# Performance work log

Hardware: AMD Instinct MI355X
Metric: run time of the kernel (lower is better)

## Reference

```python
import jax, jax.numpy as jnp
import numpy as np

N_NODES = 100000
IN_DIM = 128
HIDDEN = 256
N_CLASSES = 16
N_EDGES = 1600000
N_GRAPHS = 64


def setup_inputs() -> dict:
    key = jax.random.key(0)
    ks = jax.random.split(key, 12)
    x = jax.random.normal(ks[0], (N_NODES, IN_DIM), dtype=jnp.float32)
    edge_index = jax.random.randint(ks[1], (2, N_EDGES), 0, N_NODES, dtype=jnp.int64)
    batch = jnp.sort(jax.random.randint(ks[2], (N_NODES,), 0, N_GRAPHS, dtype=jnp.int64))
    s = 0.05
    # SAGEConv layer 1: lin_l (on aggregated neighbors, with bias), lin_r (on root, no bias)
    W1l = jax.random.normal(ks[3], (IN_DIM, HIDDEN), dtype=jnp.float32) * s
    b1 = jnp.zeros((HIDDEN,), dtype=jnp.float32)
    W1r = jax.random.normal(ks[4], (IN_DIM, HIDDEN), dtype=jnp.float32) * s
    # SAGEConv layer 2
    W2l = jax.random.normal(ks[5], (HIDDEN, HIDDEN), dtype=jnp.float32) * s
    b2 = jnp.zeros((HIDDEN,), dtype=jnp.float32)
    W2r = jax.random.normal(ks[6], (HIDDEN, HIDDEN), dtype=jnp.float32) * s
    # final classifier
    fcW = jax.random.normal(ks[7], (HIDDEN, N_CLASSES), dtype=jnp.float32) * s
    fcb = jnp.zeros((N_CLASSES,), dtype=jnp.float32)
    return {"x": x, "edge_index": edge_index, "batch": batch,
            "W1l": W1l, "b1": b1, "W1r": W1r,
            "W2l": W2l, "b2": b2, "W2r": W2r,
            "fcW": fcW, "fcb": fcb}


def _sage_conv(x, src, dst, Wl, bl, Wr, n_nodes):
    # mean aggregation of neighbor features onto destination nodes
    agg = jax.ops.segment_sum(x[src], dst, num_segments=n_nodes)      # [N, d]
    deg = jax.ops.segment_sum(jnp.ones(src.shape, x.dtype), dst, num_segments=n_nodes)
    mean = agg / jnp.maximum(deg, 1.0)[:, None]
    # out = lin_l(mean_neighbors) + lin_r(x_root)  (PyG SAGEConv, mean aggr)
    return mean @ Wl + bl + x @ Wr


def reference(x, edge_index, batch, W1l, b1, W1r, W2l, b2, W2r, fcW, fcb):
    src, dst = edge_index[0], edge_index[1]
    h = jax.nn.relu(_sage_conv(x, src, dst, W1l, b1, W1r, N_NODES))
    # dropout is identity in inference mode
    h = jax.nn.relu(_sage_conv(h, src, dst, W2l, b2, W2r, N_NODES))
    # global mean pool over graphs in the batch
    g_sum = jax.ops.segment_sum(h, batch, num_segments=N_GRAPHS)      # [G, d]
    g_cnt = jax.ops.segment_sum(jnp.ones(batch.shape, h.dtype), batch, num_segments=N_GRAPHS)
    g = g_sum / jnp.maximum(g_cnt, 1.0)[:, None]
    return g @ fcW + fcb                                              # [G, num_classes]
```

## Files before the change

kernel.cpp:

```cpp
#include <hip/hip_runtime.h>

#define INDIM 128
#define HID 256
#define NCLS 16
#define NGRAPH 64
#define CHUNK 8192

typedef __bf16 bf16_t;
typedef bf16_t bf16x8 __attribute__((ext_vector_type(8)));
typedef float f32x4 __attribute__((ext_vector_type(4)));

__device__ __forceinline__ float bfu_lo(unsigned v) {
    union { unsigned i; float f; } u; u.i = v << 16; return u.f;
}
__device__ __forceinline__ float bfu_hi(unsigned v) {
    union { unsigned i; float f; } u; u.i = v & 0xffff0000u; return u.f;
}
__device__ __forceinline__ unsigned short f2bf(float f) {
    union { float f; unsigned i; } u; u.f = f;
    unsigned b = u.i;
    return (unsigned short)((b + 0x7fffu + ((b >> 16) & 1u)) >> 16);
}

typedef __attribute__((address_space(1))) const unsigned gu32_t;
typedef __attribute__((address_space(3))) unsigned lu32_t;
__device__ __forceinline__ void gl_lds16(const void* g, void* l) {
    __builtin_amdgcn_global_load_lds((gu32_t*)g, (lu32_t*)l, 16, 0, 0);
}

__global__ void hist_kernel(const int* __restrict__ dst, int* __restrict__ deg, int E) {
    int e = blockIdx.x * blockDim.x + threadIdx.x;
    if (e < E) atomicAdd(&deg[dst[e]], 1);
}

__global__ void scan1_kernel(const int* __restrict__ deg, int* __restrict__ bsum, int n) {
    __shared__ int s[256];
    int t = threadIdx.x;
    int i = blockIdx.x * 256 + t;
    s[t] = (i < n) ? deg[i] : 0;
    __syncthreads();
    for (int off = 128; off > 0; off >>= 1) {
        if (t < off) s[t] += s[t + off];
        __syncthreads();
    }
    if (t == 0) bsum[blockIdx.x] = s[0];
}

__global__ void scan2_kernel(int* bsum, int nb) {
    __shared__ int s[1024];
    int t = threadIdx.x;
    int v = (t < nb) ? bsum[t] : 0;
    s[t] = v;
    __syncthreads();
    for (int off = 1; off < 1024; off <<= 1) {
        int u = (t >= off) ? s[t - off] : 0;
        __syncthreads();
        s[t] += u;
        __syncthreads();
    }
    if (t < nb) bsum[t] = s[t] - v;
}

__global__ void scan3_kernel(const int* __restrict__ deg, const int* __restrict__ bsum,
                             int* __restrict__ offs, int n) {
    __shared__ int s[256];
    int t = threadIdx.x;
    int i = blockIdx.x * 256 + t;
    int v = (i < n) ? deg[i] : 0;
    s[t] = v;
    __syncthreads();
    for (int off = 1; off < 256; off <<= 1) {
        int u = (t >= off) ? s[t - off] : 0;
        __syncthreads();
        s[t] += u;
        __syncthreads();
    }
    if (i < n) offs[i] = s[t] - v + bsum[blockIdx.x];
}

__global__ void initcur_kernel(const int* __restrict__ offs, int* __restrict__ gcur, int nbuck) {
    int t = blockIdx.x * blockDim.x + threadIdx.x;
    if (t < nbuck) gcur[t] = offs[t << 8];
}

__global__ __launch_bounds__(256) void binA_kernel(const int* __restrict__ src,
                                                   const int* __restrict__ dst,
                                                   int* __restrict__ gcur,
                                                   unsigned* __restrict__ tmp,
                                                   int E, int nbuck) {
    __shared__ int hist[512];
    __shared__ int base[512];
    int t = threadIdx.x;
    int e0 = blockIdx.x * CHUNK;
    int e1 = min(e0 + CHUNK, E);
    for (int i = t; i < nbuck; i += 256) hist[i] = 0;
    __syncthreads();
    for (int e = e0 + t; e < e1; e += 256) atomicAdd(&hist[dst[e] >> 8], 1);
    __syncthreads();
    for (int i = t; i < nbuck; i += 256) {
        int c = hist[i];
        base[i] = (c > 0) ? atomicAdd(&gcur[i], c) : 0;
    }
    __syncthreads();
    for (int e = e0 + t; e < e1; e += 256) {
        int d = dst[e];
        int p = atomicAdd(&base[d >> 8], 1);
        tmp[p] = ((unsigned)(d & 255) << 17) | (unsigned)src[e];
    }
}

__global__ __launch_bounds__(256) void binB_kernel(const unsigned* __restrict__ tmp,
                                                   const int* __restrict__ offs,
                                                   int* __restrict__ srclist, int E, int n) {
    __shared__ int cur[256];
    int b = blockIdx.x;
    int node0 = b << 8;
    int nnodes = min(256, n - node0);
    int t = threadIdx.x;
    if (t < nnodes) cur[t] = offs[node0 + t];
    __syncthreads();
    int ebeg = offs[node0];
    int eend = (node0 + 256 < n) ? offs[node0 + 256] : E;
    for (int e = ebeg + t; e < eend; e += 256) {
        unsigned v = tmp[e];
        int p = atomicAdd(&cur[v >> 17], 1);
        srclist[p] = (int)(v & 0x1FFFFu);
    }
}

__global__ void cast_x_kernel(const float* __restrict__ x, unsigned short* __restrict__ xb,
                              int total4) {
    int idx = blockIdx.x * blockDim.x + threadIdx.x;
    if (idx >= total4) return;
    int i4 = idx * 4;
    float4 v = *(const float4*)(x + i4);
    *(ushort4*)(xb + i4) = make_ushort4(f2bf(v.x), f2bf(v.y), f2bf(v.z), f2bf(v.w));
}

__global__ void wcast1_kernel(const float* __restrict__ Wl, const float* __restrict__ Wr,
                              unsigned short* __restrict__ Bt) {
    int idx = blockIdx.x * blockDim.x + threadIdx.x;
    int n = idx >> 8, k = idx & 255;
    float v = (k < 128) ? Wl[(size_t)k * 256 + n] : Wr[(size_t)(k - 128) * 256 + n];
    Bt[(size_t)n * 256 + k] = f2bf(v);
}

__global__ void wcast2_kernel(const float* __restrict__ Wl, const float* __restrict__ Wr,
                              unsigned short* __restrict__ Bt) {
    int idx = blockIdx.x * blockDim.x + threadIdx.x;
    int n = idx >> 9, k = idx & 511;
    float v = (k < 256) ? Wl[(size_t)k * 256 + n] : Wr[(size_t)(k - 256) * 256 + n];
    Bt[(size_t)n * 512 + k] = f2bf(v);
}

__global__ void agg1_kernel(const unsigned short* __restrict__ xb, const int* __restrict__ srclist,
                            const int* __restrict__ offs, const int* __restrict__ deg,
                            unsigned short* __restrict__ mean, int n) {
    int gid = blockIdx.x * blockDim.x + threadIdx.x;
    int node = gid >> 6, lane = gid & 63;
    if (node >= n) return;
    int st = offs[node], d = deg[node], end = st + d;
    float a0 = 0.f, a1 = 0.f, b0 = 0.f, b1 = 0.f;
    float c0 = 0.f, c1 = 0.f, d0 = 0.f, d1 = 0.f;
    int e = st;
    for (; e + 3 < end; e += 4) {
        int s0 = srclist[e], s1 = srclist[e + 1], s2 = srclist[e + 2], s3 = srclist[e + 3];
        unsigned v0 = *(const unsigned*)(xb + (size_t)s0 * 128 + lane * 2);
        unsigned v1 = *(const unsigned*)(xb + (size_t)s1 * 128 + lane * 2);
        unsigned v2 = *(const unsigned*)(xb + (size_t)s2 * 128 + lane * 2);
        unsigned v3 = *(const unsigned*)(xb + (size_t)s3 * 128 + lane * 2);
        a0 += bfu_lo(v0); a1 += bfu_hi(v0);
        b0 += bfu_lo(v1); b1 += bfu_hi(v1);
        c0 += bfu_lo(v2); c1 += bfu_hi(v2);
        d0 += bfu_lo(v3); d1 += bfu_hi(v3);
    }
    for (; e < end; ++e) {
        unsigned v0 = *(const unsigned*)(xb + (size_t)srclist[e] * 128 + lane * 2);
        a0 += bfu_lo(v0); a1 += bfu_hi(v0);
    }
    float inv = 1.f / fmaxf((float)d, 1.f);
    ushort2 o = make_ushort2(f2bf(((a0 + b0) + (c0 + d0)) * inv),
                             f2bf(((a1 + b1) + (c1 + d1)) * inv));
    *(ushort2*)(mean + (size_t)node * 128 + lane * 2) = o;
}

__global__ void agg2_kernel(const unsigned short* __restrict__ h1, const int* __restrict__ srclist,
                            const int* __restrict__ offs, const int* __restrict__ deg,
                            unsigned short* __restrict__ mean, int n) {
    int gid = blockIdx.x * blockDim.x + threadIdx.x;
    int node = gid >> 6, lane = gid & 63;
    if (node >= n) return;
    int st = offs[node], d = deg[node], end = st + d;
    float a0 = 0, a1 = 0, a2 = 0, a3 = 0, b0 = 0, b1 = 0, b2 = 0, b3 = 0;
    float c0 = 0, c1 = 0, c2 = 0, c3 = 0, e0 = 0, e1 = 0, e2 = 0, e3 = 0;
    int e = st;
    for (; e + 3 < end; e += 4) {
        int s0 = srclist[e], s1 = srclist[e + 1], s2 = srclist[e + 2], s3 = srclist[e + 3];
        uint2 v0 = *(const uint2*)(h1 + (size_t)s0 * 256 + lane * 4);
        uint2 v1 = *(const uint2*)(h1 + (size_t)s1 * 256 + lane * 4);
        uint2 v2 = *(const uint2*)(h1 + (size_t)s2 * 256 + lane * 4);
        uint2 v3 = *(const uint2*)(h1 + (size_t)s3 * 256 + lane * 4);
        a0 += bfu_lo(v0.x); a1 += bfu_hi(v0.x); a2 += bfu_lo(v0.y); a3 += bfu_hi(v0.y);
        b0 += bfu_lo(v1.x); b1 += bfu_hi(v1.x); b2 += bfu_lo(v1.y); b3 += bfu_hi(v1.y);
        c0 += bfu_lo(v2.x); c1 += bfu_hi(v2.x); c2 += bfu_lo(v2.y); c3 += bfu_hi(v2.y);
        e0 += bfu_lo(v3.x); e1 += bfu_hi(v3.x); e2 += bfu_lo(v3.y); e3 += bfu_hi(v3.y);
    }
    for (; e < end; ++e) {
        uint2 v0 = *(const uint2*)(h1 + (size_t)srclist[e] * 256 + lane * 4);
        a0 += bfu_lo(v0.x); a1 += bfu_hi(v0.x); a2 += bfu_lo(v0.y); a3 += bfu_hi(v0.y);
    }
    float inv = 1.f / fmaxf((float)d, 1.f);
    ushort4 o = make_ushort4(f2bf(((a0 + b0) + (c0 + e0)) * inv),
                             f2bf(((a1 + b1) + (c1 + e1)) * inv),
                             f2bf(((a2 + b2) + (c2 + e2)) * inv),
                             f2bf(((a3 + b3) + (c3 + e3)) * inv));
    *(ushort4*)(mean + (size_t)node * 256 + lane * 4) = o;
}

template <int KH>
__global__ __launch_bounds__(256) void gemm_kernel(
        const bf16_t* __restrict__ A1, const bf16_t* __restrict__ A2,
        const bf16_t* __restrict__ Bt, const float* __restrict__ bias,
        unsigned short* __restrict__ H, int M) {
    constexpr int KT = 2 * KH;
    constexpr int NC = KT / 64;
    constexpr int CPH = KH / 64;
    __shared__ unsigned short As[64 * 64];
    int t = threadIdx.x, wave = t >> 6, lane = t & 63;
    int quad = lane >> 4, l16 = lane & 15;
    int row0 = blockIdx.x * 64, n0 = wave * 64;

    f32x4 acc[4][4];
#pragma unroll
    for (int i = 0; i < 4; ++i)
#pragma unroll
        for (int j = 0; j < 4; ++j) acc[i][j] = (f32x4)(0.f);

    int rA = wave * 8 + (lane >> 3);
    int kb = lane & 7;
    int kswA = (kb ^ (rA & 7)) << 3;
    unsigned short* ldsA = &As[(size_t)(wave * 8) * 64];
    unsigned short* ldsB = &As[(size_t)(32 + wave * 8) * 64];

    const bf16_t* Bp = Bt + (size_t)(n0 + l16) * KT + quad * 8;

    for (int c = 0; c < NC; ++c) {
        const bf16_t* Ah = (c < CPH) ? A1 : A2;
        int kk = ((c < CPH) ? c : (c - CPH)) * 64;
        gl_lds16(Ah + (size_t)(row0 + rA) * KH + kk + kswA, ldsA);
        gl_lds16(Ah + (size_t)(row0 + 32 + rA) * KH + kk + kswA, ldsB);
        __syncthreads();
        int bk = c * 64;
#pragma unroll
        for (int sub = 0; sub < 2; ++sub) {
            bf16x8 af[4], bfr[4];
#pragma unroll
            for (int mi = 0; mi < 4; ++mi) {
                int r = mi * 16 + l16;
                int qb = sub * 4 + quad;
                af[mi] = *(const bf16x8*)&As[r * 64 + ((qb ^ (r & 7)) << 3)];
            }
#pragma unroll
            for (int ni = 0; ni < 4; ++ni)
                bfr[ni] = *(const bf16x8*)(Bp + (size_t)(ni * 16) * KT + bk + sub * 32);
#pragma unroll
            for (int mi = 0; mi < 4; ++mi)
#pragma unroll
                for (int ni = 0; ni < 4; ++ni)
                    acc[mi][ni] = __builtin_amdgcn_mfma_f32_16x16x32_bf16(
                        af[mi], bfr[ni], acc[mi][ni], 0, 0, 0);
        }
        __syncthreads();
    }

    float bv[4];
#pragma unroll
    for (int ni = 0; ni < 4; ++ni) bv[ni] = bias[n0 + ni * 16 + l16];
#pragma unroll
    for (int mi = 0; mi < 4; ++mi) {
#pragma unroll
        for (int r = 0; r < 4; ++r) {
            int row = row0 + mi * 16 + quad * 4 + r;
            if (row < M) {
#pragma unroll
                for (int ni = 0; ni < 4; ++ni) {
                    int col = n0 + ni * 16 + l16;
                    H[(size_t)row * 256 + col] = f2bf(fmaxf(acc[mi][ni][r] + bv[ni], 0.f));
                }
            }
        }
    }
}

__global__ void pool_kernel(const unsigned short* __restrict__ h2, const int* __restrict__ batch,
                            float* __restrict__ g, float* __restrict__ cnt, int n) {
    int col = threadIdx.x;
    int row0 = blockIdx.x * 256;
    float acc = 0.f;
    int cur = -1, seglen = 0;
    for (int r = 0; r < 256; ++r) {
        int row = row0 + r;
        if (row >= n) break;
        int b = batch[row];
        if (b != cur) {
            if (cur >= 0) {
                atomicAdd(&g[cur * 256 + col], acc);
                if (col == 0) atomicAdd(&cnt[cur], (float)seglen);
            }
            acc = 0.f; cur = b; seglen = 0;
        }
        union { unsigned i; float f; } u;
        u.i = ((unsigned)h2[(size_t)row * 256 + col]) << 16;
        acc += u.f;
        seglen++;
    }
    if (cur >= 0) {
        atomicAdd(&g[cur * 256 + col], acc);
        if (col == 0) atomicAdd(&cnt[cur], (float)seglen);
    }
}

__global__ void final_kernel(const float* __restrict__ g, const float* __restrict__ cnt,
                             const float* __restrict__ fcW, const float* __restrict__ fcb,
                             float* __restrict__ out) {
    int t = threadIdx.x;
    for (int o = t; o < NGRAPH * NCLS; o += 256) {
        int gi = o >> 4, c = o & 15;
        float inv = 1.f / fmaxf(cnt[gi], 1.f);
        float dot = 0.f;
        for (int k = 0; k < 256; ++k) dot += g[gi * 256 + k] * fcW[k * 16 + c];
        out[o] = dot * inv + fcb[c];
    }
}

extern "C" void kernel_launch(void* const* d_in, const int* in_sizes, int n_in, void* d_out,
                              int out_size, void* d_ws, size_t ws_size, hipStream_t stream) {
    const float* x   = (const float*)d_in[0];
    const int* edge  = (const int*)d_in[1];
    const int* batch = (const int*)d_in[2];
    const float* W1l = (const float*)d_in[3];
    const float* b1  = (const float*)d_in[4];
    const float* W1r = (const float*)d_in[5];
    const float* W2l = (const float*)d_in[6];
    const float* b2  = (const float*)d_in[7];
    const float* W2r = (const float*)d_in[8];
    const float* fcW = (const float*)d_in[9];
    const float* fcb = (const float*)d_in[10];
    float* out = (float*)d_out;

    const int n = in_sizes[0] / INDIM;
    const int E = in_sizes[1] / 2;
    const int* src = edge;
    const int* dst = edge + E;
    const int nbuck = (n + 255) >> 8;

    char* ws = (char*)d_ws;
    size_t off = 0;
    auto alloc = [&](size_t bytes) {
        size_t p = off;
        off = (off + bytes + 511) & ~(size_t)511;
        return p;
    };
    size_t offs_o    = alloc((size_t)n * 4);
    size_t deg_o     = alloc((size_t)n * 4);
    size_t cnt_o     = alloc(64 * 4);
    size_t g_o       = alloc(64 * 256 * 4);
    size_t zero_end  = off;
    size_t bsum_o    = alloc(1024 * 4);
    size_t gcur_o    = alloc(512 * 4);
    size_t srclist_o = alloc((size_t)E * 4);
    size_t bt1_o     = alloc(256 * 256 * 2);
    size_t bt2_o     = alloc(256 * 512 * 2);
    size_t xbm2_o    = alloc((size_t)n * 256 * 2);
    size_t mean1_o   = alloc((size_t)n * 128 * 2);
    size_t h1_o      = alloc((size_t)n * 256 * 2);
    size_t h2_o      = alloc((size_t)n * 256 * 2);

    int*   offs    = (int*)(ws + offs_o);
    int*   deg     = (int*)(ws + deg_o);
    float* cnt     = (float*)(ws + cnt_o);
    float* g       = (float*)(ws + g_o);
    int*   bsum    = (int*)(ws + bsum_o);
    int*   gcur    = (int*)(ws + gcur_o);
    int*   srclist = (int*)(ws + srclist_o);
    unsigned short* Bt1   = (unsigned short*)(ws + bt1_o);
    unsigned short* Bt2   = (unsigned short*)(ws + bt2_o);
    unsigned short* xb16  = (unsigned short*)(ws + xbm2_o);
    unsigned short* mean2 = (unsigned short*)(ws + xbm2_o);
    unsigned short* mean1 = (unsigned short*)(ws + mean1_o);
    unsigned short* h1b   = (unsigned short*)(ws + h1_o);
    unsigned*       tmp   = (unsigned*)(ws + h2_o);
    unsigned short* h2b   = (unsigned short*)(ws + h2_o);

    hipMemsetAsync(ws + deg_o, 0, zero_end - deg_o, stream);

    int eb = (E + 255) / 256;
    int nb = (n + 255) / 256;
    hist_kernel<<<eb, 256, 0, stream>>>(dst, deg, E);
    scan1_kernel<<<nb, 256, 0, stream>>>(deg, bsum, n);
    scan2_kernel<<<1, 1024, 0, stream>>>(bsum, nb);
    scan3_kernel<<<nb, 256, 0, stream>>>(deg, bsum, offs, n);
    initcur_kernel<<<(nbuck + 255) / 256, 256, 0, stream>>>(offs, gcur, nbuck);
    binA_kernel<<<(E + CHUNK - 1) / CHUNK, 256, 0, stream>>>(src, dst, gcur, tmp, E, nbuck);
    binB_kernel<<<nbuck, 256, 0, stream>>>(tmp, offs, srclist, E, n);

    cast_x_kernel<<<(n * INDIM / 4 + 255) / 256, 256, 0, stream>>>(x, xb16, n * INDIM / 4);
    wcast1_kernel<<<256, 256, 0, stream>>>(W1l, W1r, Bt1);
    wcast2_kernel<<<512, 256, 0, stream>>>(W2l, W2r, Bt2);

    int aggb = (n * 64 + 255) / 256;
    int gemmb = (n + 63) / 64;

    agg1_kernel<<<aggb, 256, 0, stream>>>(xb16, srclist, offs, deg, mean1, n);
    gemm_kernel<128><<<gemmb, 256, 0, stream>>>(
        (const bf16_t*)mean1, (const bf16_t*)xb16, (const bf16_t*)Bt1, b1, h1b, n);
    agg2_kernel<<<aggb, 256, 0, stream>>>(h1b, srclist, offs, deg, mean2, n);
    gemm_kernel<256><<<gemmb, 256, 0, stream>>>(
        (const bf16_t*)mean2, (const bf16_t*)h1b, (const bf16_t*)Bt2, b2, h2b, n);

    pool_kernel<<<nb, 256, 0, stream>>>(h2b, batch, g, cnt, n);
    final_kernel<<<1, 256, 0, stream>>>(g, cnt, fcW, fcb, out);
}
```

Measured before the change: 662.5 us.

## Widen neighbor gathers to 16-byte loads and merge small prep kernels

The aggregation kernels now split each wavefront into lane groups that each load a full 16-byte slice of a different neighbor row, then combine the partial sums with cross-lane shuffles. This cuts the number of gather instructions issued per edge and raises the bytes moved per load. The node offset and degree are made wave-uniform with readfirstlane. Separately, the cursor-init kernel is folded into scan3, and the three cast kernels are merged into one launch to save launch overhead. The trade-off is extra shuffle work, and some lane groups sit idle on the tail edges of low-degree nodes.

```diff
diff --git a/kernel.cpp b/kernel.cpp
--- a/kernel.cpp
+++ b/kernel.cpp
@@ -21,6 +21,9 @@
     unsigned b = u.i;
     return (unsigned short)((b + 0x7fffu + ((b >> 16) & 1u)) >> 16);
 }
+__device__ __forceinline__ unsigned packbf(float lo, float hi) {
+    return (unsigned)f2bf(lo) | ((unsigned)f2bf(hi) << 16);
+}
 
 typedef __attribute__((address_space(1))) const unsigned gu32_t;
 typedef __attribute__((address_space(3))) unsigned lu32_t;
@@ -28,6 +31,14 @@
     __builtin_amdgcn_global_load_lds((gu32_t*)g, (lu32_t*)l, 16, 0, 0);
 }
 
+#define ACC8(a, v)                                   \
+    do {                                             \
+        a[0] += bfu_lo((v).x); a[1] += bfu_hi((v).x); \
+        a[2] += bfu_lo((v).y); a[3] += bfu_hi((v).y); \
+        a[4] += bfu_lo((v).z); a[5] += bfu_hi((v).z); \
+        a[6] += bfu_lo((v).w); a[7] += bfu_hi((v).w); \
+    } while (0)
+
 __global__ void hist_kernel(const int* __restrict__ dst, int* __restrict__ deg, int E) {
     int e = blockIdx.x * blockDim.x + threadIdx.x;
     if (e < E) atomicAdd(&deg[dst[e]], 1);
@@ -62,7 +73,7 @@
 }
 
 __global__ void scan3_kernel(const int* __restrict__ deg, const int* __restrict__ bsum,
-                             int* __restrict__ offs, int n) {
+                             int* __restrict__ offs, int* __restrict__ gcur, int n) {
     __shared__ int s[256];
     int t = threadIdx.x;
     int i = blockIdx.x * 256 + t;
@@ -76,11 +87,7 @@
         __syncthreads();
     }
     if (i < n) offs[i] = s[t] - v + bsum[blockIdx.x];
-}
-
-__global__ void initcur_kernel(const int* __restrict__ offs, int* __restrict__ gcur, int nbuck) {
-    int t = blockIdx.x * blockDim.x + threadIdx.x;
-    if (t < nbuck) gcur[t] = offs[t << 8];
+    if (t == 0) gcur[blockIdx.x] = bsum[blockIdx.x];
 }
 
 __global__ __launch_bounds__(256) void binA_kernel(const int* __restrict__ src,
@@ -128,29 +135,27 @@
     }
 }
 
-__global__ void cast_x_kernel(const float* __restrict__ x, unsigned short* __restrict__ xb,
-                              int total4) {
-    int idx = blockIdx.x * blockDim.x + threadIdx.x;
-    if (idx >= total4) return;
-    int i4 = idx * 4;
-    float4 v = *(const float4*)(x + i4);
-    *(ushort4*)(xb + i4) = make_ushort4(f2bf(v.x), f2bf(v.y), f2bf(v.z), f2bf(v.w));
-}
-
-__global__ void wcast1_kernel(const float* __restrict__ Wl, const float* __restrict__ Wr,
-                              unsigned short* __restrict__ Bt) {
-    int idx = blockIdx.x * blockDim.x + threadIdx.x;
-    int n = idx >> 8, k = idx & 255;
-    float v = (k < 128) ? Wl[(size_t)k * 256 + n] : Wr[(size_t)(k - 128) * 256 + n];
-    Bt[(size_t)n * 256 + k] = f2bf(v);
-}
-
-__global__ void wcast2_kernel(const float* __restrict__ Wl, const float* __restrict__ Wr,
-                              unsigned short* __restrict__ Bt) {
-    int idx = blockIdx.x * blockDim.x + threadIdx.x;
-    int n = idx >> 9, k = idx & 511;
-    float v = (k < 256) ? Wl[(size_t)k * 256 + n] : Wr[(size_t)(k - 256) * 256 + n];
-    Bt[(size_t)n * 512 + k] = f2bf(v);
+__global__ void prep_kernel(const float* __restrict__ x, unsigned short* __restrict__ xb,
+                            const float* __restrict__ W1l, const float* __restrict__ W1r,
+                            unsigned short* __restrict__ Bt1,
+                            const float* __restrict__ W2l, const float* __restrict__ W2r,
+                            unsigned short* __restrict__ Bt2, int castb) {
+    int b = blockIdx.x, t = threadIdx.x;
+    if (b < castb) {
+        int i4 = (b * 256 + t) * 4;
+        float4 v = *(const float4*)(x + i4);
+        *(ushort4*)(xb + i4) = make_ushort4(f2bf(v.x), f2bf(v.y), f2bf(v.z), f2bf(v.w));
+    } else if (b < castb + 256) {
+        int idx = (b - castb) * 256 + t;
+        int nn = idx >> 8, k = idx & 255;
+        float v = (k < 128) ? W1l[(size_t)k * 256 + nn] : W1r[(size_t)(k - 128) * 256 + nn];
+        Bt1[(size_t)nn * 256 + k] = f2bf(v);
+    } else {
+        int idx = (b - castb - 256) * 256 + t;
+        int nn = idx >> 9, k = idx & 511;
+        float v = (k < 256) ? W2l[(size_t)k * 256 + nn] : W2r[(size_t)(k - 256) * 256 + nn];
+        Bt2[(size_t)nn * 512 + k] = f2bf(v);
+    }
 }
 
 __global__ void agg1_kernel(const unsigned short* __restrict__ xb, const int* __restrict__ srclist,
@@ -159,29 +164,49 @@
     int gid = blockIdx.x * blockDim.x + threadIdx.x;
     int node = gid >> 6, lane = gid & 63;
     if (node >= n) return;
-    int st = offs[node], d = deg[node], end = st + d;
-    float a0 = 0.f, a1 = 0.f, b0 = 0.f, b1 = 0.f;
-    float c0 = 0.f, c1 = 0.f, d0 = 0.f, d1 = 0.f;
+    int q = lane >> 4, sub = lane & 15;
+    int st = __builtin_amdgcn_readfirstlane(offs[node]);
+    int d = __builtin_amdgcn_readfirstlane(deg[node]);
+    int end = st + d;
+    float aA[8] = {0, 0, 0, 0, 0, 0, 0, 0}, aB[8] = {0, 0, 0, 0, 0, 0, 0, 0};
+    const unsigned short* rb = xb + sub * 8;
     int e = st;
+    for (; e + 7 < end; e += 8) {
+        int s0 = srclist[e + q];
+        int s1 = srclist[e + 4 + q];
+        uint4 v0 = *(const uint4*)(rb + (size_t)s0 * 128);
+        uint4 v1 = *(const uint4*)(rb + (size_t)s1 * 128);
+        ACC8(aA, v0);
+        ACC8(aB, v1);
+    }
     for (; e + 3 < end; e += 4) {
-        int s0 = srclist[e], s1 = srclist[e + 1], s2 = srclist[e + 2], s3 = srclist[e + 3];
-        unsigned v0 = *(const unsigned*)(xb + (size_t)s0 * 128 + lane * 2);
-        unsigned v1 = *(const unsigned*)(xb + (size_t)s1 * 128 + lane * 2);
-        unsigned v2 = *(const unsigned*)(xb + (size_t)s2 * 128 + lane * 2);
-        unsigned v3 = *(const unsigned*)(xb + (size_t)s3 * 128 + lane * 2);
-        a0 += bfu_lo(v0); a1 += bfu_hi(v0);
-        b0 += bfu_lo(v1); b1 += bfu_hi(v1);
-        c0 += bfu_lo(v2); c1 += bfu_hi(v2);
-        d0 += bfu_lo(v3); d1 += bfu_hi(v3);
-    }
-    for (; e < end; ++e) {
-        unsigned v0 = *(const unsigned*)(xb + (size_t)srclist[e] * 128 + lane * 2);
-        a0 += bfu_lo(v0); a1 += bfu_hi(v0);
+        int s0 = srclist[e + q];
+        uint4 v0 = *(const uint4*)(rb + (size_t)s0 * 128);
+        ACC8(aA, v0);
+    }
+    int rem = end - e;
+    if (rem > 0) {
+        int s0 = srclist[e + ((q < rem) ? q : 0)];
+        uint4 v0 = *(const uint4*)(rb + (size_t)s0 * 128);
+        if (q < rem) ACC8(aA, v0);
     }
     float inv = 1.f / fmaxf((float)d, 1.f);
-    ushort2 o = make_ushort2(f2bf(((a0 + b0) + (c0 + d0)) * inv),
-                             f2bf(((a1 + b1) + (c1 + d1)) * inv));
-    *(ushort2*)(mean + (size_t)node * 128 + lane * 2) = o;
+    float tot[8];
+#pragma unroll
+    for (int i = 0; i < 8; ++i) {
+        float s = aA[i] + aB[i];
+        s += __shfl_xor(s, 16);
+        s += __shfl_xor(s, 32);
+        tot[i] = s * inv;
+    }
+    if (lane < 16) {
+        uint4 o;
+        o.x = packbf(tot[0], tot[1]);
+        o.y = packbf(tot[2], tot[3]);
+        o.z = packbf(tot[4], tot[5]);
+        o.w = packbf(tot[6], tot[7]);
+        *(uint4*)(mean + (size_t)node * 128 + sub * 8) = o;
+    }
 }
 
 __global__ void agg2_kernel(const unsigned short* __restrict__ h1, const int* __restrict__ srclist,
@@ -190,31 +215,54 @@
     int gid = blockIdx.x * blockDim.x + threadIdx.x;
     int node = gid >> 6, lane = gid & 63;
     if (node >= n) return;
-    int st = offs[node], d = deg[node], end = st + d;
-    float a0 = 0, a1 = 0, a2 = 0, a3 = 0, b0 = 0, b1 = 0, b2 = 0, b3 = 0;
-    float c0 = 0, c1 = 0, c2 = 0, c3 = 0, e0 = 0, e1 = 0, e2 = 0, e3 = 0;
+    int half = lane >> 5, sub = lane & 31;
+    int st = __builtin_amdgcn_readfirstlane(offs[node]);
+    int d = __builtin_amdgcn_readfirstlane(deg[node]);
+    int end = st + d;
+    float aA[8] = {0, 0, 0, 0, 0, 0, 0, 0}, aB[8] = {0, 0, 0, 0, 0, 0, 0, 0};
+    float aC[8] = {0, 0, 0, 0, 0, 0, 0, 0}, aD[8] = {0, 0, 0, 0, 0, 0, 0, 0};
+    const unsigned short* rb = h1 + sub * 8;
     int e = st;
-    for (; e + 3 < end; e += 4) {
-        int s0 = srclist[e], s1 = srclist[e + 1], s2 = srclist[e + 2], s3 = srclist[e + 3];
-        uint2 v0 = *(const uint2*)(h1 + (size_t)s0 * 256 + lane * 4);
-        uint2 v1 = *(const uint2*)(h1 + (size_t)s1 * 256 + lane * 4);
-        uint2 v2 = *(const uint2*)(h1 + (size_t)s2 * 256 + lane * 4);
-        uint2 v3 = *(const uint2*)(h1 + (size_t)s3 * 256 + lane * 4);
-        a0 += bfu_lo(v0.x); a1 += bfu_hi(v0.x); a2 += bfu_lo(v0.y); a3 += bfu_hi(v0.y);
-        b0 += bfu_lo(v1.x); b1 += bfu_hi(v1.x); b2 += bfu_lo(v1.y); b3 += bfu_hi(v1.y);
-        c0 += bfu_lo(v2.x); c1 += bfu_hi(v2.x); c2 += bfu_lo(v2.y); c3 += bfu_hi(v2.y);
-        e0 += bfu_lo(v3.x); e1 += bfu_hi(v3.x); e2 += bfu_lo(v3.y); e3 += bfu_hi(v3.y);
-    }
-    for (; e < end; ++e) {
-        uint2 v0 = *(const uint2*)(h1 + (size_t)srclist[e] * 256 + lane * 4);
-        a0 += bfu_lo(v0.x); a1 += bfu_hi(v0.x); a2 += bfu_lo(v0.y); a3 += bfu_hi(v0.y);
+    for (; e + 7 < end; e += 8) {
+        int s0 = srclist[e + half];
+        int s1 = srclist[e + 2 + half];
+        int s2 = srclist[e + 4 + half];
+        int s3 = srclist[e + 6 + half];
+        uint4 v0 = *(const uint4*)(rb + (size_t)s0 * 256);
+        uint4 v1 = *(const uint4*)(rb + (size_t)s1 * 256);
+        uint4 v2 = *(const uint4*)(rb + (size_t)s2 * 256);
+        uint4 v3 = *(const uint4*)(rb + (size_t)s3 * 256);
+        ACC8(aA, v0);
+        ACC8(aB, v1);
+        ACC8(aC, v2);
+        ACC8(aD, v3);
+    }
+    for (; e + 1 < end; e += 2) {
+        int s0 = srclist[e + half];
+        uint4 v0 = *(const uint4*)(rb + (size_t)s0 * 256);
+        ACC8(aA, v0);
+    }
+    if (e < end) {
+        int s0 = srclist[e];
+        uint4 v0 = *(const uint4*)(rb + (size_t)s0 * 256);
+        if (half == 0) ACC8(aA, v0);
     }
     float inv = 1.f / fmaxf((float)d, 1.f);
-    ushort4 o = make_ushort4(f2bf(((a0 + b0) + (c0 + e0)) * inv),
-                             f2bf(((a1 + b1) + (c1 + e1)) * inv),
-                             f2bf(((a2 + b2) + (c2 + e2)) * inv),
-                             f2bf(((a3 + b3) + (c3 + e3)) * inv));
-    *(ushort4*)(mean + (size_t)node * 256 + lane * 4) = o;
+    float tot[8];
+#pragma unroll
+    for (int i = 0; i < 8; ++i) {
+        float s = (aA[i] + aB[i]) + (aC[i] + aD[i]);
+        s += __shfl_xor(s, 32);
+        tot[i] = s * inv;
+    }
+    if (half == 0) {
+        uint4 o;
+        o.x = packbf(tot[0], tot[1]);
+        o.y = packbf(tot[2], tot[3]);
+        o.z = packbf(tot[4], tot[5]);
+        o.w = packbf(tot[6], tot[7]);
+        *(uint4*)(mean + (size_t)node * 256 + sub * 8) = o;
+    }
 }
 
 template <int KH>
@@ -399,14 +447,12 @@
     hist_kernel<<<eb, 256, 0, stream>>>(dst, deg, E);
     scan1_kernel<<<nb, 256, 0, stream>>>(deg, bsum, n);
     scan2_kernel<<<1, 1024, 0, stream>>>(bsum, nb);
-    scan3_kernel<<<nb, 256, 0, stream>>>(deg, bsum, offs, n);
-    initcur_kernel<<<(nbuck + 255) / 256, 256, 0, stream>>>(offs, gcur, nbuck);
+    scan3_kernel<<<nb, 256, 0, stream>>>(deg, bsum, offs, gcur, n);
     binA_kernel<<<(E + CHUNK - 1) / CHUNK, 256, 0, stream>>>(src, dst, gcur, tmp, E, nbuck);
     binB_kernel<<<nbuck, 256, 0, stream>>>(tmp, offs, srclist, E, n);
 
-    cast_x_kernel<<<(n * INDIM / 4 + 255) / 256, 256, 0, stream>>>(x, xb16, n * INDIM / 4);
-    wcast1_kernel<<<256, 256, 0, stream>>>(W1l, W1r, Bt1);
-    wcast2_kernel<<<512, 256, 0, stream>>>(W2l, W2r, Bt2);
+    int castb = n * INDIM / 4 / 256;
+    prep_kernel<<<castb + 256 + 512, 256, 0, stream>>>(x, xb16, W1l, W1r, Bt1, W2l, W2r, Bt2, castb);
 
     int aggb = (n * 64 + 255) / 256;
     int gemmb = (n + 63) / 64;
```

After: 641.5 us. -3.2%, faster.
